# Optimization experiments

Hardware: AMD Instinct MI355X
Metric: run time of the kernel (lower is better)

Reference implementation:

```python
import jax, jax.numpy as jnp
import numpy as np

NH = 8       # num attention heads (hardcoded in module)
NL = 6       # n_layers
EPS = 1e-5   # LayerNorm eps (torch default)


def pos_enc(dim, length):
    # faithful to module's positional_encoding: even cols sin, odd cols cos,
    # with angle = pos / 10000^(2i/dim) where i indexes ALL columns via arange(0,2*dim,2)/dim
    pos = jnp.arange(length, dtype=jnp.float32)[:, None]
    div = 1.0 / (10000.0 ** (jnp.arange(0, 2 * dim, 2, dtype=jnp.float32) / dim))
    ang = pos * div[None, :]  # [length, dim]
    cols = jnp.arange(dim)
    return jnp.where(cols % 2 == 0, jnp.sin(ang), jnp.cos(ang))


def layernorm(x):
    m = x.mean(-1, keepdims=True)
    v = x.var(-1, keepdims=True)  # biased, matches torch LayerNorm
    return (x - m) / jnp.sqrt(v + EPS)


def setup_inputs() -> dict:
    key = jax.random.key(0)
    ks = jax.random.split(key, 8)
    S, H = 2048, 1024
    D = H // NH
    sc = 1.0 / np.sqrt(H)  # ~ torch Linear init scale
    return {
        "inputs": jax.random.normal(ks[0], (S, H), jnp.float32),
        "Wq": jax.random.normal(ks[1], (NH, H, D), jnp.float32) * sc,
        "bq": jnp.zeros((NH, D), jnp.float32),
        "Wk": jax.random.normal(ks[2], (NH, H, D), jnp.float32) * sc,
        "bk": jnp.zeros((NH, D), jnp.float32),
        "Wv": jax.random.normal(ks[3], (NH, H, D), jnp.float32) * sc,
        "bv": jnp.zeros((NH, D), jnp.float32),
        "W1": jax.random.normal(ks[4], (H, H), jnp.float32) * sc,
        "b1": jnp.zeros((H,), jnp.float32),
        "W2": jax.random.normal(ks[5], (H, H), jnp.float32) * sc,
        "b2": jnp.zeros((H,), jnp.float32),
    }


def reference(inputs, Wq, bq, Wk, bk, Wv, bv, W1, b1, W2, b2):
    S, H = inputs.shape
    scale = jnp.sqrt(jnp.float32(H))  # module scales by sqrt(hidden), not sqrt(head_dim)
    x = inputs + pos_enc(H, S)        # [S, H]
    kv = x  # dropout in eval mode = identity; k_v_input fixed to layer-0 input (faithful)
    # K/V are identical every layer (shared weights + fixed kv input)
    K = jnp.einsum('sh,nhd->nsd', kv, Wk) + bk[:, None, :]  # [NH, S, D]
    V = jnp.einsum('sh,nhd->nsd', kv, Wv) + bv[:, None, :]
    t_in = x
    for _ in range(NL):
        Q = jnp.einsum('sh,nhd->nsd', t_in, Wq) + bq[:, None, :]
        A = jax.nn.softmax(jnp.einsum('nsd,ntd->nst', Q, K) / scale, axis=-1)
        ctx = jnp.einsum('nst,ntd->nsd', A, V)        # [NH, S, D]
        cat = ctx.transpose(1, 0, 2).reshape(S, H)    # concat heads on feature dim
        mh = layernorm(t_in + cat)
        ff = jax.nn.relu(mh @ W1 + b1) @ W2 + b2
        t_in = layernorm(mh + ff)
    return t_in
```

## Files before the change

kernel.cpp:

```cpp
#include <hip/hip_runtime.h>

#define S_LEN 2048
#define H_DIM 1024
#define NHEAD 8
#define D_HEAD 128
#define KSPLIT 4
#define KV_PER (S_LEN / KSPLIT)

typedef __bf16 bf16x8 __attribute__((ext_vector_type(8)));
typedef float floatx4 __attribute__((ext_vector_type(4)));

__device__ __forceinline__ float b2f(unsigned short u) {
    union { unsigned int i; float f; } v;
    v.i = ((unsigned int)u) << 16;
    return v.f;
}
__device__ __forceinline__ unsigned short f2b(float f) {
    union { float f; unsigned int i; } v;
    v.f = f;
    return (unsigned short)((v.i + 0x7fffu + ((v.i >> 16) & 1u)) >> 16);
}

__device__ __forceinline__ void dma16(void* lds, const void* g) {
    __builtin_amdgcn_global_load_lds(
        (const __attribute__((address_space(1))) void*)g,
        (__attribute__((address_space(3))) void*)lds, 16, 0, 0);
}

__global__ __launch_bounds__(256) void posenc_kernel(
    const float* __restrict__ in, float* __restrict__ xf,
    unsigned short* __restrict__ xb)
{
    int g = blockIdx.x * 256 + threadIdx.x;
    int s = g >> 10;
    int h = g & 1023;
    float dv = powf(10000.0f, -(float)h * (1.0f / 512.0f));
    float ang = (float)s * dv;
    float pe = (h & 1) ? cosf(ang) : sinf(ang);
    float x = in[g] + pe;
    xf[g] = x;
    xb[g] = f2b(x);
}

__global__ __launch_bounds__(256) void transpose_f2b(
    const float* __restrict__ in, unsigned short* __restrict__ out, int R, int C)
{
    __shared__ unsigned short tile[32][33];
    const float* ih = in + (size_t)blockIdx.z * R * C;
    unsigned short* oh = out + (size_t)blockIdx.z * R * C;
    int r0 = blockIdx.y * 32, c0 = blockIdx.x * 32;
    int tx = threadIdx.x, ty = threadIdx.y;
    for (int i = ty; i < 32; i += 8)
        tile[i][tx] = f2b(ih[(size_t)(r0 + i) * C + c0 + tx]);
    __syncthreads();
    for (int i = ty; i < 32; i += 8)
        oh[(size_t)(c0 + i) * R + r0 + tx] = tile[tx][i];
}

template <int MODE, bool RELU>
__global__ __launch_bounds__(256, 4) void gemm_bt(
    const unsigned short* __restrict__ A, const unsigned short* __restrict__ Bt,
    const float* __restrict__ bias, float* __restrict__ Cf,
    unsigned short* __restrict__ Cb, int M, int N, int K, int ldt)
{
    __shared__ __align__(16) unsigned short sA[2][64 * 64];
    __shared__ __align__(16) unsigned short sB[2][64 * 64];
    const int tid = threadIdx.x;
    const int wave = tid >> 6, lane = tid & 63;
    const int quad = lane >> 4, l16 = lane & 15;
    const int i0 = blockIdx.y * 64, j0 = blockIdx.x * 64;
    const int wm = (wave >> 1) * 32, wn = (wave & 1) * 32;

    const int srow = lane >> 3;
    const int schunk = (lane & 7) ^ (srow & 7);
    const unsigned short* Ap0 = A + (size_t)(i0 + wave * 8 + srow) * K + schunk * 8;
    const unsigned short* Ap1 = A + (size_t)(i0 + 32 + wave * 8 + srow) * K + schunk * 8;
    const unsigned short* Bp0 = Bt + (size_t)(j0 + wave * 8 + srow) * K + schunk * 8;
    const unsigned short* Bp1 = Bt + (size_t)(j0 + 32 + wave * 8 + srow) * K + schunk * 8;
    const int ld0 = (wave * 8) * 64, ld1 = (32 + wave * 8) * 64;

    floatx4 z4 = {0.f, 0.f, 0.f, 0.f};
    floatx4 acc[2][2];
#pragma unroll
    for (int i = 0; i < 2; i++)
#pragma unroll
        for (int j = 0; j < 2; j++) acc[i][j] = z4;

    dma16(sA[0] + ld0, Ap0);
    dma16(sA[0] + ld1, Ap1);
    dma16(sB[0] + ld0, Bp0);
    dma16(sB[0] + ld1, Bp1);
    __syncthreads();

    int buf = 0;
    for (int k0 = 0; k0 < K; k0 += 64) {
        if (k0 + 64 < K) {
            dma16(sA[buf ^ 1] + ld0, Ap0 + k0 + 64);
            dma16(sA[buf ^ 1] + ld1, Ap1 + k0 + 64);
            dma16(sB[buf ^ 1] + ld0, Bp0 + k0 + 64);
            dma16(sB[buf ^ 1] + ld1, Bp1 + k0 + 64);
        }
        const unsigned short* cA = sA[buf];
        const unsigned short* cB = sB[buf];
#pragma unroll
        for (int kh = 0; kh < 2; kh++) {
            bf16x8 af[2], bfr[2];
#pragma unroll
            for (int mi = 0; mi < 2; mi++) {
                int row = wm + mi * 16 + l16;
                int p = (kh * 4 + quad) ^ (l16 & 7);
                af[mi] = *(const bf16x8*)(cA + row * 64 + p * 8);
            }
#pragma unroll
            for (int ni = 0; ni < 2; ni++) {
                int row = wn + ni * 16 + l16;
                int p = (kh * 4 + quad) ^ (l16 & 7);
                bfr[ni] = *(const bf16x8*)(cB + row * 64 + p * 8);
            }
#pragma unroll
            for (int mi = 0; mi < 2; mi++)
#pragma unroll
                for (int ni = 0; ni < 2; ni++)
                    acc[mi][ni] = __builtin_amdgcn_mfma_f32_16x16x32_bf16(
                        af[mi], bfr[ni], acc[mi][ni], 0, 0, 0);
        }
        __syncthreads();
        buf ^= 1;
    }

#pragma unroll
    for (int mi = 0; mi < 2; mi++) {
#pragma unroll
        for (int ni = 0; ni < 2; ni++) {
            const int col = j0 + wn + ni * 16 + l16;
            const float bval = bias[col];
#pragma unroll
            for (int r = 0; r < 4; r++) {
                const int row_o = i0 + wm + mi * 16 + quad * 4 + r;
                float v = acc[mi][ni][r] + bval;
                if (RELU) v = fmaxf(v, 0.0f);
                if (MODE == 0) Cb[(size_t)row_o * N + col] = f2b(v);
                else if (MODE == 1) Cb[(size_t)col * ldt + row_o] = f2b(v);
                else Cf[(size_t)row_o * N + col] = v;
            }
        }
    }
}

__global__ __launch_bounds__(256, 3) void flash_attn(
    const unsigned short* __restrict__ Qg, const unsigned short* __restrict__ Kg,
    const unsigned short* __restrict__ Vt, unsigned short* __restrict__ Op,
    float* __restrict__ Lp)
{
    __shared__ __align__(16) unsigned short sK[64 * 128];
    __shared__ __align__(16) unsigned short sV[128 * 64];

    const int tid = threadIdx.x;
    const int wave = tid >> 6, lane = tid & 63;
    const int quad = lane >> 4, l16 = lane & 15;
    const int head = blockIdx.y;
    const int q0 = blockIdx.x * 64;
    const int split = blockIdx.z;
    const int h0 = head * D_HEAD;

    bf16x8 aq[4];
    const int qrow = q0 + wave * 16 + l16;
#pragma unroll
    for (int ks = 0; ks < 4; ks++)
        aq[ks] = *(const bf16x8*)(Qg + (size_t)qrow * H_DIM + h0 + ks * 32 + quad * 8);

    unsigned short* myP = sK + wave * (16 * 72);

    const int k_r = wave * 4 + (lane >> 4);
    const int k_c = (lane & 15) ^ (k_r & 15);
    const int v_r = wave * 8 + (lane >> 3);
    const int v_c = (lane & 7) ^ (v_r & 7);

    const unsigned short* Kbase = Kg + h0;
    const unsigned short* Vbase = Vt + (size_t)h0 * S_LEN;
    const int kt0 = split * KV_PER;

    floatx4 z4 = {0.f, 0.f, 0.f, 0.f};
    floatx4 o[8];
#pragma unroll
    for (int i = 0; i < 8; i++) o[i] = z4;
    float l_r[4] = {0.f, 0.f, 0.f, 0.f};

    for (int it0 = 0; it0 < KV_PER; it0 += 64) {
        const int t0 = kt0 + it0;
        __syncthreads();
#pragma unroll
        for (int it = 0; it < 4; it++) {
            dma16(sK + (wave * 4 + it * 16) * 128,
                  Kbase + (size_t)(t0 + k_r + it * 16) * H_DIM + k_c * 8);
            dma16(sV + (wave * 8 + it * 32) * 64,
                  Vbase + (size_t)(v_r + it * 32) * S_LEN + t0 + v_c * 8);
        }
        __syncthreads();

        floatx4 sc[4];
#pragma unroll
        for (int ni = 0; ni < 4; ni++) {
            sc[ni] = z4;
#pragma unroll
            for (int ks = 0; ks < 4; ks++) {
                int p = (ks * 4 + quad) ^ l16;
                bf16x8 bk = *(const bf16x8*)(sK + (ni * 16 + l16) * 128 + p * 8);
                sc[ni] = __builtin_amdgcn_mfma_f32_16x16x32_bf16(aq[ks], bk, sc[ni], 0, 0, 0);
            }
        }

#pragma unroll
        for (int ni = 0; ni < 4; ni++)
#pragma unroll
            for (int r = 0; r < 4; r++) {
                float p = __expf(sc[ni][r] * 0.03125f);
                sc[ni][r] = p;
                l_r[r] += p;
            }

        __syncthreads();
#pragma unroll
        for (int ni = 0; ni < 4; ni++)
#pragma unroll
            for (int r = 0; r < 4; r++) {
                int prow = quad * 4 + r;
                myP[prow * 72 + ((ni * 16 + l16) ^ ((prow & 8) << 1))] = f2b(sc[ni][r]);
            }
        bf16x8 ap[2];
#pragma unroll
        for (int ks = 0; ks < 2; ks++)
            ap[ks] = *(const bf16x8*)(myP + l16 * 72 + ((ks * 32 + quad * 8) ^ ((l16 & 8) << 1)));
#pragma unroll
        for (int ni = 0; ni < 8; ni++) {
#pragma unroll
            for (int ks = 0; ks < 2; ks++) {
                int p = (ks * 4 + quad) ^ (l16 & 7);
                bf16x8 bv = *(const bf16x8*)(sV + (ni * 16 + l16) * 64 + p * 8);
                o[ni] = __builtin_amdgcn_mfma_f32_16x16x32_bf16(ap[ks], bv, o[ni], 0, 0, 0);
            }
        }
    }

#pragma unroll
    for (int r = 0; r < 4; r++)
#pragma unroll
        for (int off = 1; off < 16; off <<= 1)
            l_r[r] += __shfl_xor(l_r[r], off, 64);

#pragma unroll
    for (int r = 0; r < 4; r++) {
        float inv = 1.0f / l_r[r];
        int row = q0 + wave * 16 + quad * 4 + r;
#pragma unroll
        for (int ni = 0; ni < 8; ni++)
            Op[((size_t)split * S_LEN + row) * H_DIM + h0 + ni * 16 + l16] =
                f2b(o[ni][r] * inv);
        if (l16 == 0)
            Lp[(split * NHEAD + head) * S_LEN + row] = l_r[r];
    }
}

__global__ __launch_bounds__(256) void merge_add_layernorm(
    const float* __restrict__ t, const unsigned short* __restrict__ Op,
    const float* __restrict__ Lp,
    float* __restrict__ of, unsigned short* __restrict__ ob)
{
    __shared__ float red[8];
    const int row = blockIdx.x, tid = threadIdx.x;
    const int head = tid >> 5;
    const size_t base = (size_t)row * H_DIM + tid * 4;

    float l_s[KSPLIT];
    ushort4 os[KSPLIT];
#pragma unroll
    for (int sp = 0; sp < KSPLIT; sp++) {
        os[sp] = *(const ushort4*)(Op + ((size_t)sp * S_LEN + row) * H_DIM + tid * 4);
        l_s[sp] = Lp[(sp * NHEAD + head) * S_LEN + row];
    }
    float W = 0.f, a0 = 0.f, a1 = 0.f, a2 = 0.f, a3 = 0.f;
#pragma unroll
    for (int sp = 0; sp < KSPLIT; sp++) {
        float w = l_s[sp];
        W += w;
        a0 += w * b2f(os[sp].x);
        a1 += w * b2f(os[sp].y);
        a2 += w * b2f(os[sp].z);
        a3 += w * b2f(os[sp].w);
    }
    float inv = 1.0f / W;
    float4 x = *(const float4*)(t + base);
    float v0 = x.x + a0 * inv, v1 = x.y + a1 * inv;
    float v2 = x.z + a2 * inv, v3 = x.w + a3 * inv;

    float s = v0 + v1 + v2 + v3;
    float q = v0 * v0 + v1 * v1 + v2 * v2 + v3 * v3;
#pragma unroll
    for (int off = 32; off >= 1; off >>= 1) {
        s += __shfl_xor(s, off, 64);
        q += __shfl_xor(q, off, 64);
    }
    if ((tid & 63) == 0) { red[tid >> 6] = s; red[4 + (tid >> 6)] = q; }
    __syncthreads();
    s = red[0] + red[1] + red[2] + red[3];
    q = red[4] + red[5] + red[6] + red[7];
    const float mean = s * (1.0f / (float)H_DIM);
    const float var = q * (1.0f / (float)H_DIM) - mean * mean;
    const float rstd = rsqrtf(var + 1e-5f);
    float o0 = (v0 - mean) * rstd, o1 = (v1 - mean) * rstd;
    float o2 = (v2 - mean) * rstd, o3 = (v3 - mean) * rstd;
    *(float4*)(of + base) = make_float4(o0, o1, o2, o3);
    *(ushort4*)(ob + base) = make_ushort4(f2b(o0), f2b(o1), f2b(o2), f2b(o3));
}

__global__ __launch_bounds__(256) void add_layernorm(
    const float* __restrict__ a, const float* __restrict__ b,
    float* __restrict__ of, unsigned short* __restrict__ ob)
{
    __shared__ float red[8];
    const int row = blockIdx.x, tid = threadIdx.x;
    const size_t base = (size_t)row * H_DIM + tid * 4;
    float4 x = *(const float4*)(a + base);
    float4 y = *(const float4*)(b + base);
    float v0 = x.x + y.x, v1 = x.y + y.y, v2 = x.z + y.z, v3 = x.w + y.w;
    float s = v0 + v1 + v2 + v3;
    float q = v0 * v0 + v1 * v1 + v2 * v2 + v3 * v3;
#pragma unroll
    for (int off = 32; off >= 1; off >>= 1) {
        s += __shfl_xor(s, off, 64);
        q += __shfl_xor(q, off, 64);
    }
    if ((tid & 63) == 0) { red[tid >> 6] = s; red[4 + (tid >> 6)] = q; }
    __syncthreads();
    s = red[0] + red[1] + red[2] + red[3];
    q = red[4] + red[5] + red[6] + red[7];
    const float mean = s * (1.0f / (float)H_DIM);
    const float var = q * (1.0f / (float)H_DIM) - mean * mean;
    const float rstd = rsqrtf(var + 1e-5f);
    float o0 = (v0 - mean) * rstd, o1 = (v1 - mean) * rstd;
    float o2 = (v2 - mean) * rstd, o3 = (v3 - mean) * rstd;
    *(float4*)(of + base) = make_float4(o0, o1, o2, o3);
    *(ushort4*)(ob + base) = make_ushort4(f2b(o0), f2b(o1), f2b(o2), f2b(o3));
}

extern "C" void kernel_launch(void* const* d_in, const int* in_sizes, int n_in,
                              void* d_out, int out_size, void* d_ws, size_t ws_size,
                              hipStream_t stream)
{
    (void)in_sizes; (void)n_in; (void)out_size; (void)ws_size;
    const float* in = (const float*)d_in[0];
    const float* Wq = (const float*)d_in[1];
    const float* bq = (const float*)d_in[2];
    const float* Wk = (const float*)d_in[3];
    const float* bk = (const float*)d_in[4];
    const float* Wv = (const float*)d_in[5];
    const float* bv = (const float*)d_in[6];
    const float* W1 = (const float*)d_in[7];
    const float* b1 = (const float*)d_in[8];
    const float* W2 = (const float*)d_in[9];
    const float* b2 = (const float*)d_in[10];

    char* ws = (char*)d_ws;
    const size_t MB = 1024 * 1024;
    float* t_f32 = (float*)(ws + 0 * MB);
    float* cf_f32 = (float*)(ws + 8 * MB);
    unsigned short* t_b = (unsigned short*)(ws + 16 * MB);
    unsigned short* K_b = (unsigned short*)(ws + 20 * MB);
    unsigned short* Vt_b = (unsigned short*)(ws + 24 * MB);
    unsigned short* Q_b = (unsigned short*)(ws + 28 * MB);
    unsigned short* WqT = (unsigned short*)(ws + 32 * MB);
    unsigned short* WkT = (unsigned short*)(ws + 34 * MB);
    unsigned short* WvT = (unsigned short*)(ws + 36 * MB);
    unsigned short* W1T = (unsigned short*)(ws + 38 * MB);
    unsigned short* W2T = (unsigned short*)(ws + 40 * MB);
    unsigned short* Op = (unsigned short*)(ws + 42 * MB);
    float* Lp = (float*)(ws + 58 * MB);

    dim3 tb(32, 8);
    transpose_f2b<<<dim3(4, 32, 8), tb, 0, stream>>>(Wq, WqT, H_DIM, D_HEAD);
    transpose_f2b<<<dim3(4, 32, 8), tb, 0, stream>>>(Wk, WkT, H_DIM, D_HEAD);
    transpose_f2b<<<dim3(4, 32, 8), tb, 0, stream>>>(Wv, WvT, H_DIM, D_HEAD);
    transpose_f2b<<<dim3(32, 32, 1), tb, 0, stream>>>(W1, W1T, H_DIM, H_DIM);
    transpose_f2b<<<dim3(32, 32, 1), tb, 0, stream>>>(W2, W2T, H_DIM, H_DIM);

    posenc_kernel<<<(S_LEN * H_DIM) / 256, 256, 0, stream>>>(in, t_f32, t_b);

    dim3 gg(H_DIM / 64, S_LEN / 64);
    gemm_bt<0, false><<<gg, 256, 0, stream>>>(t_b, WkT, bk, nullptr, K_b, S_LEN, H_DIM, H_DIM, 0);
    gemm_bt<1, false><<<gg, 256, 0, stream>>>(t_b, WvT, bv, nullptr, Vt_b, S_LEN, H_DIM, H_DIM, S_LEN);

    for (int layer = 0; layer < 6; layer++) {
        gemm_bt<0, false><<<gg, 256, 0, stream>>>(t_b, WqT, bq, nullptr, Q_b, S_LEN, H_DIM, H_DIM, 0);
        flash_attn<<<dim3(S_LEN / 64, NHEAD, KSPLIT), 256, 0, stream>>>(Q_b, K_b, Vt_b, Op, Lp);
        merge_add_layernorm<<<S_LEN, 256, 0, stream>>>(t_f32, Op, Lp, t_f32, t_b);
        gemm_bt<0, true><<<gg, 256, 0, stream>>>(t_b, W1T, b1, nullptr, Q_b, S_LEN, H_DIM, H_DIM, 0);
        gemm_bt<2, false><<<gg, 256, 0, stream>>>(Q_b, W2T, b2, cf_f32, nullptr, S_LEN, H_DIM, H_DIM, 0);
        float* of = (layer == 5) ? (float*)d_out : t_f32;
        add_layernorm<<<S_LEN, 256, 0, stream>>>(t_f32, cf_f32, of, t_b);
    }
}
```

Before: 633.0 us.

## Process two 16-row query tiles per wave in flash attention to reuse K/V tiles

Each wave now handles 32 query rows instead of 16, so a block covers 128 queries, and every K/V fragment read from LDS feeds two MFMAs. The grid halves along the query dimension. P now goes to its own LDS buffer instead of aliasing sK, which removes one __syncthreads per KV tile. In exchange, register pressure roughly doubles for accumulators, occupancy drops from 3 to 2 blocks per CU, there are fewer blocks (512) to fill the GPU, and LDS use per block grows.

```diff
diff --git a/kernel.cpp b/kernel.cpp
--- a/kernel.cpp
+++ b/kernel.cpp
@@ -147,29 +147,33 @@
     }
 }
 
-__global__ __launch_bounds__(256, 3) void flash_attn(
+__global__ __launch_bounds__(256, 2) void flash_attn(
     const unsigned short* __restrict__ Qg, const unsigned short* __restrict__ Kg,
     const unsigned short* __restrict__ Vt, unsigned short* __restrict__ Op,
     float* __restrict__ Lp)
 {
     __shared__ __align__(16) unsigned short sK[64 * 128];
     __shared__ __align__(16) unsigned short sV[128 * 64];
+    __shared__ __align__(16) unsigned short sP[4 * 32 * 72];
 
     const int tid = threadIdx.x;
     const int wave = tid >> 6, lane = tid & 63;
     const int quad = lane >> 4, l16 = lane & 15;
     const int head = blockIdx.y;
-    const int q0 = blockIdx.x * 64;
+    const int q0 = blockIdx.x * 128;
     const int split = blockIdx.z;
     const int h0 = head * D_HEAD;
 
-    bf16x8 aq[4];
-    const int qrow = q0 + wave * 16 + l16;
-#pragma unroll
-    for (int ks = 0; ks < 4; ks++)
-        aq[ks] = *(const bf16x8*)(Qg + (size_t)qrow * H_DIM + h0 + ks * 32 + quad * 8);
-
-    unsigned short* myP = sK + wave * (16 * 72);
+    bf16x8 aq[2][4];
+#pragma unroll
+    for (int m = 0; m < 2; m++) {
+        const int qrow = q0 + wave * 32 + m * 16 + l16;
+#pragma unroll
+        for (int ks = 0; ks < 4; ks++)
+            aq[m][ks] = *(const bf16x8*)(Qg + (size_t)qrow * H_DIM + h0 + ks * 32 + quad * 8);
+    }
+
+    unsigned short* myP = sP + wave * (32 * 72);
 
     const int k_r = wave * 4 + (lane >> 4);
     const int k_c = (lane & 15) ^ (k_r & 15);
@@ -181,10 +185,12 @@
     const int kt0 = split * KV_PER;
 
     floatx4 z4 = {0.f, 0.f, 0.f, 0.f};
-    floatx4 o[8];
-#pragma unroll
-    for (int i = 0; i < 8; i++) o[i] = z4;
-    float l_r[4] = {0.f, 0.f, 0.f, 0.f};
+    floatx4 o[2][8];
+#pragma unroll
+    for (int m = 0; m < 2; m++)
+#pragma unroll
+        for (int i = 0; i < 8; i++) o[m][i] = z4;
+    float l_r[2][4] = {{0.f, 0.f, 0.f, 0.f}, {0.f, 0.f, 0.f, 0.f}};
 
     for (int it0 = 0; it0 < KV_PER; it0 += 64) {
         const int t0 = kt0 + it0;
@@ -198,67 +204,86 @@
         }
         __syncthreads();
 
-        floatx4 sc[4];
+        floatx4 sc[2][4];
+#pragma unroll
+        for (int m = 0; m < 2; m++)
+#pragma unroll
+            for (int ni = 0; ni < 4; ni++) sc[m][ni] = z4;
 #pragma unroll
         for (int ni = 0; ni < 4; ni++) {
-            sc[ni] = z4;
 #pragma unroll
             for (int ks = 0; ks < 4; ks++) {
                 int p = (ks * 4 + quad) ^ l16;
                 bf16x8 bk = *(const bf16x8*)(sK + (ni * 16 + l16) * 128 + p * 8);
-                sc[ni] = __builtin_amdgcn_mfma_f32_16x16x32_bf16(aq[ks], bk, sc[ni], 0, 0, 0);
+#pragma unroll
+                for (int m = 0; m < 2; m++)
+                    sc[m][ni] = __builtin_amdgcn_mfma_f32_16x16x32_bf16(
+                        aq[m][ks], bk, sc[m][ni], 0, 0, 0);
             }
         }
 
 #pragma unroll
-        for (int ni = 0; ni < 4; ni++)
-#pragma unroll
-            for (int r = 0; r < 4; r++) {
-                float p = __expf(sc[ni][r] * 0.03125f);
-                sc[ni][r] = p;
-                l_r[r] += p;
-            }
-
-        __syncthreads();
-#pragma unroll
-        for (int ni = 0; ni < 4; ni++)
-#pragma unroll
-            for (int r = 0; r < 4; r++) {
-                int prow = quad * 4 + r;
-                myP[prow * 72 + ((ni * 16 + l16) ^ ((prow & 8) << 1))] = f2b(sc[ni][r]);
-            }
-        bf16x8 ap[2];
-#pragma unroll
-        for (int ks = 0; ks < 2; ks++)
-            ap[ks] = *(const bf16x8*)(myP + l16 * 72 + ((ks * 32 + quad * 8) ^ ((l16 & 8) << 1)));
+        for (int m = 0; m < 2; m++)
+#pragma unroll
+            for (int ni = 0; ni < 4; ni++)
+#pragma unroll
+                for (int r = 0; r < 4; r++) {
+                    float p = __expf(sc[m][ni][r] * 0.03125f);
+                    sc[m][ni][r] = p;
+                    l_r[m][r] += p;
+                }
+
+#pragma unroll
+        for (int m = 0; m < 2; m++)
+#pragma unroll
+            for (int ni = 0; ni < 4; ni++)
+#pragma unroll
+                for (int r = 0; r < 4; r++) {
+                    int prow = m * 16 + quad * 4 + r;
+                    myP[prow * 72 + ((ni * 16 + l16) ^ ((prow & 8) << 1))] = f2b(sc[m][ni][r]);
+                }
+        bf16x8 ap[2][2];
+#pragma unroll
+        for (int m = 0; m < 2; m++)
+#pragma unroll
+            for (int ks = 0; ks < 2; ks++)
+                ap[m][ks] = *(const bf16x8*)(myP + (m * 16 + l16) * 72 +
+                                             ((ks * 32 + quad * 8) ^ ((l16 & 8) << 1)));
 #pragma unroll
         for (int ni = 0; ni < 8; ni++) {
 #pragma unroll
             for (int ks = 0; ks < 2; ks++) {
                 int p = (ks * 4 + quad) ^ (l16 & 7);
                 bf16x8 bv = *(const bf16x8*)(sV + (ni * 16 + l16) * 64 + p * 8);
-                o[ni] = __builtin_amdgcn_mfma_f32_16x16x32_bf16(ap[ks], bv, o[ni], 0, 0, 0);
+#pragma unroll
+                for (int m = 0; m < 2; m++)
+                    o[m][ni] = __builtin_amdgcn_mfma_f32_16x16x32_bf16(
+                        ap[m][ks], bv, o[m][ni], 0, 0, 0);
             }
         }
     }
 
 #pragma unroll
-    for (int r = 0; r < 4; r++)
-#pragma unroll
-        for (int off = 1; off < 16; off <<= 1)
-            l_r[r] += __shfl_xor(l_r[r], off, 64);
-
-#pragma unroll
-    for (int r = 0; r < 4; r++) {
-        float inv = 1.0f / l_r[r];
-        int row = q0 + wave * 16 + quad * 4 + r;
-#pragma unroll
-        for (int ni = 0; ni < 8; ni++)
-            Op[((size_t)split * S_LEN + row) * H_DIM + h0 + ni * 16 + l16] =
-                f2b(o[ni][r] * inv);
-        if (l16 == 0)
-            Lp[(split * NHEAD + head) * S_LEN + row] = l_r[r];
-    }
+    for (int m = 0; m < 2; m++)
+#pragma unroll
+        for (int r = 0; r < 4; r++)
+#pragma unroll
+            for (int off = 1; off < 16; off <<= 1)
+                l_r[m][r] += __shfl_xor(l_r[m][r], off, 64);
+
+#pragma unroll
+    for (int m = 0; m < 2; m++)
+#pragma unroll
+        for (int r = 0; r < 4; r++) {
+            float inv = 1.0f / l_r[m][r];
+            int row = q0 + wave * 32 + m * 16 + quad * 4 + r;
+#pragma unroll
+            for (int ni = 0; ni < 8; ni++)
+                Op[((size_t)split * S_LEN + row) * H_DIM + h0 + ni * 16 + l16] =
+                    f2b(o[m][ni][r] * inv);
+            if (l16 == 0)
+                Lp[(split * NHEAD + head) * S_LEN + row] = l_r[m][r];
+        }
 }
 
 __global__ __launch_bounds__(256) void merge_add_layernorm(
@@ -391,7 +416,7 @@
 
     for (int layer = 0; layer < 6; layer++) {
         gemm_bt<0, false><<<gg, 256, 0, stream>>>(t_b, WqT, bq, nullptr, Q_b, S_LEN, H_DIM, H_DIM, 0);
-        flash_attn<<<dim3(S_LEN / 64, NHEAD, KSPLIT), 256, 0, stream>>>(Q_b, K_b, Vt_b, Op, Lp);
+        flash_attn<<<dim3(S_LEN / 128, NHEAD, KSPLIT), 256, 0, stream>>>(Q_b, K_b, Vt_b, Op, Lp);
         merge_add_layernorm<<<S_LEN, 256, 0, stream>>>(t_f32, Op, Lp, t_f32, t_b);
         gemm_bt<0, true><<<gg, 256, 0, stream>>>(t_b, W1T, b1, nullptr, Q_b, S_LEN, H_DIM, H_DIM, 0);
         gemm_bt<2, false><<<gg, 256, 0, stream>>>(Q_b, W2T, b2, cf_f32, nullptr, S_LEN, H_DIM, H_DIM, 0);
```

Result: no change. 630.3 us (-0.4%).

## Double-buffer V tiles in LDS and load K fragments directly from global

Applied to the files above, without the earlier changes.

The flash attention kernel now stages V tiles into two LDS buffers, prefetching the next tile while computing on the current one, and leaves one barrier per iteration. K is no longer staged in LDS: each wave reads its K fragments straight from global memory into registers. P gets its own LDS region. This aims to hide load latency and cut barriers. The cost is redundant global K reads across the four waves and uncoalesced row-strided accesses.

```diff
diff --git a/kernel.cpp b/kernel.cpp
--- a/kernel.cpp
+++ b/kernel.cpp
@@ -152,8 +152,8 @@
     const unsigned short* __restrict__ Vt, unsigned short* __restrict__ Op,
     float* __restrict__ Lp)
 {
-    __shared__ __align__(16) unsigned short sK[64 * 128];
-    __shared__ __align__(16) unsigned short sV[128 * 64];
+    __shared__ __align__(16) unsigned short sV[2][128 * 64];
+    __shared__ __align__(16) unsigned short sP[4 * 16 * 72];
 
     const int tid = threadIdx.x;
     const int wave = tid >> 6, lane = tid & 63;
@@ -169,10 +169,8 @@
     for (int ks = 0; ks < 4; ks++)
         aq[ks] = *(const bf16x8*)(Qg + (size_t)qrow * H_DIM + h0 + ks * 32 + quad * 8);
 
-    unsigned short* myP = sK + wave * (16 * 72);
-
-    const int k_r = wave * 4 + (lane >> 4);
-    const int k_c = (lane & 15) ^ (k_r & 15);
+    unsigned short* myP = sP + wave * (16 * 72);
+
     const int v_r = wave * 8 + (lane >> 3);
     const int v_c = (lane & 7) ^ (v_r & 7);
 
@@ -186,28 +184,35 @@
     for (int i = 0; i < 8; i++) o[i] = z4;
     float l_r[4] = {0.f, 0.f, 0.f, 0.f};
 
+#pragma unroll
+    for (int it = 0; it < 4; it++)
+        dma16(sV[0] + (wave * 8 + it * 32) * 64,
+              Vbase + (size_t)(v_r + it * 32) * S_LEN + kt0 + v_c * 8);
+    __syncthreads();
+
+    int buf = 0;
     for (int it0 = 0; it0 < KV_PER; it0 += 64) {
         const int t0 = kt0 + it0;
-        __syncthreads();
-#pragma unroll
-        for (int it = 0; it < 4; it++) {
-            dma16(sK + (wave * 4 + it * 16) * 128,
-                  Kbase + (size_t)(t0 + k_r + it * 16) * H_DIM + k_c * 8);
-            dma16(sV + (wave * 8 + it * 32) * 64,
-                  Vbase + (size_t)(v_r + it * 32) * S_LEN + t0 + v_c * 8);
-        }
-        __syncthreads();
+        if (it0 + 64 < KV_PER) {
+            const int nt = t0 + 64;
+#pragma unroll
+            for (int it = 0; it < 4; it++)
+                dma16(sV[buf ^ 1] + (wave * 8 + it * 32) * 64,
+                      Vbase + (size_t)(v_r + it * 32) * S_LEN + nt + v_c * 8);
+        }
 
         floatx4 sc[4];
 #pragma unroll
         for (int ni = 0; ni < 4; ni++) {
+            bf16x8 bkf[4];
+#pragma unroll
+            for (int ks = 0; ks < 4; ks++)
+                bkf[ks] = *(const bf16x8*)(Kbase +
+                    (size_t)(t0 + ni * 16 + l16) * H_DIM + ks * 32 + quad * 8);
             sc[ni] = z4;
 #pragma unroll
-            for (int ks = 0; ks < 4; ks++) {
-                int p = (ks * 4 + quad) ^ l16;
-                bf16x8 bk = *(const bf16x8*)(sK + (ni * 16 + l16) * 128 + p * 8);
-                sc[ni] = __builtin_amdgcn_mfma_f32_16x16x32_bf16(aq[ks], bk, sc[ni], 0, 0, 0);
-            }
+            for (int ks = 0; ks < 4; ks++)
+                sc[ni] = __builtin_amdgcn_mfma_f32_16x16x32_bf16(aq[ks], bkf[ks], sc[ni], 0, 0, 0);
         }
 
 #pragma unroll
@@ -219,7 +224,6 @@
                 l_r[r] += p;
             }
 
-        __syncthreads();
 #pragma unroll
         for (int ni = 0; ni < 4; ni++)
 #pragma unroll
@@ -231,15 +235,19 @@
 #pragma unroll
         for (int ks = 0; ks < 2; ks++)
             ap[ks] = *(const bf16x8*)(myP + l16 * 72 + ((ks * 32 + quad * 8) ^ ((l16 & 8) << 1)));
+
 #pragma unroll
         for (int ni = 0; ni < 8; ni++) {
 #pragma unroll
             for (int ks = 0; ks < 2; ks++) {
                 int p = (ks * 4 + quad) ^ (l16 & 7);
-                bf16x8 bv = *(const bf16x8*)(sV + (ni * 16 + l16) * 64 + p * 8);
+                bf16x8 bv = *(const bf16x8*)(sV[buf] + (ni * 16 + l16) * 64 + p * 8);
                 o[ni] = __builtin_amdgcn_mfma_f32_16x16x32_bf16(ap[ks], bv, o[ni], 0, 0, 0);
             }
         }
+
+        __syncthreads();
+        buf ^= 1;
     }
 
 #pragma unroll
```

After: 976.7 us. +54.3%, slower.

## Double-buffer K/V tiles in flash attention with smaller 32-key tiles

Applied to the files above, without the earlier changes.

Restructures the flash attention inner loop to prefetch the next K/V tile into a second LDS buffer while computing on the current one. The KV tile shrinks from 64 to 32 keys so that two buffers fit, and a dedicated P scratch buffer replaces the reuse of sK. This cuts the per-iteration barrier count from three to one and overlaps global-to-LDS DMA with MFMA work. In exchange there are twice as many loop iterations, and the async DMA now relies on the end-of-loop barrier for completion.

```diff
diff --git a/kernel.cpp b/kernel.cpp
--- a/kernel.cpp
+++ b/kernel.cpp
@@ -152,8 +152,9 @@
     const unsigned short* __restrict__ Vt, unsigned short* __restrict__ Op,
     float* __restrict__ Lp)
 {
-    __shared__ __align__(16) unsigned short sK[64 * 128];
-    __shared__ __align__(16) unsigned short sV[128 * 64];
+    __shared__ __align__(16) unsigned short sK[2][32 * 128];
+    __shared__ __align__(16) unsigned short sV[2][128 * 32];
+    __shared__ __align__(16) unsigned short sP[4 * 16 * 40];
 
     const int tid = threadIdx.x;
     const int wave = tid >> 6, lane = tid & 63;
@@ -169,12 +170,12 @@
     for (int ks = 0; ks < 4; ks++)
         aq[ks] = *(const bf16x8*)(Qg + (size_t)qrow * H_DIM + h0 + ks * 32 + quad * 8);
 
-    unsigned short* myP = sK + wave * (16 * 72);
+    unsigned short* myP = sP + wave * (16 * 40);
 
     const int k_r = wave * 4 + (lane >> 4);
     const int k_c = (lane & 15) ^ (k_r & 15);
-    const int v_r = wave * 8 + (lane >> 3);
-    const int v_c = (lane & 7) ^ (v_r & 7);
+    const int v_r = wave * 16 + (lane >> 2);
+    const int v_c = (lane & 3) ^ (v_r & 3);
 
     const unsigned short* Kbase = Kg + h0;
     const unsigned short* Vbase = Vt + (size_t)h0 * S_LEN;
@@ -186,32 +187,42 @@
     for (int i = 0; i < 8; i++) o[i] = z4;
     float l_r[4] = {0.f, 0.f, 0.f, 0.f};
 
-    for (int it0 = 0; it0 < KV_PER; it0 += 64) {
-        const int t0 = kt0 + it0;
-        __syncthreads();
-#pragma unroll
-        for (int it = 0; it < 4; it++) {
-            dma16(sK + (wave * 4 + it * 16) * 128,
-                  Kbase + (size_t)(t0 + k_r + it * 16) * H_DIM + k_c * 8);
-            dma16(sV + (wave * 8 + it * 32) * 64,
-                  Vbase + (size_t)(v_r + it * 32) * S_LEN + t0 + v_c * 8);
-        }
-        __syncthreads();
-
-        floatx4 sc[4];
-#pragma unroll
-        for (int ni = 0; ni < 4; ni++) {
+#pragma unroll
+    for (int it = 0; it < 2; it++) {
+        dma16(sK[0] + (it * 16 + wave * 4) * 128,
+              Kbase + (size_t)(kt0 + k_r + it * 16) * H_DIM + k_c * 8);
+        dma16(sV[0] + (it * 64 + wave * 16) * 32,
+              Vbase + (size_t)(v_r + it * 64) * S_LEN + kt0 + v_c * 8);
+    }
+    __syncthreads();
+
+    int buf = 0;
+    for (int it0 = 0; it0 < KV_PER; it0 += 32) {
+        if (it0 + 32 < KV_PER) {
+            const int nt = kt0 + it0 + 32;
+#pragma unroll
+            for (int it = 0; it < 2; it++) {
+                dma16(sK[buf ^ 1] + (it * 16 + wave * 4) * 128,
+                      Kbase + (size_t)(nt + k_r + it * 16) * H_DIM + k_c * 8);
+                dma16(sV[buf ^ 1] + (it * 64 + wave * 16) * 32,
+                      Vbase + (size_t)(v_r + it * 64) * S_LEN + nt + v_c * 8);
+            }
+        }
+
+        floatx4 sc[2];
+#pragma unroll
+        for (int ni = 0; ni < 2; ni++) {
             sc[ni] = z4;
 #pragma unroll
             for (int ks = 0; ks < 4; ks++) {
                 int p = (ks * 4 + quad) ^ l16;
-                bf16x8 bk = *(const bf16x8*)(sK + (ni * 16 + l16) * 128 + p * 8);
+                bf16x8 bk = *(const bf16x8*)(sK[buf] + (ni * 16 + l16) * 128 + p * 8);
                 sc[ni] = __builtin_amdgcn_mfma_f32_16x16x32_bf16(aq[ks], bk, sc[ni], 0, 0, 0);
             }
         }
 
 #pragma unroll
-        for (int ni = 0; ni < 4; ni++)
+        for (int ni = 0; ni < 2; ni++)
 #pragma unroll
             for (int r = 0; r < 4; r++) {
                 float p = __expf(sc[ni][r] * 0.03125f);
@@ -219,27 +230,24 @@
                 l_r[r] += p;
             }
 
-        __syncthreads();
-#pragma unroll
-        for (int ni = 0; ni < 4; ni++)
+#pragma unroll
+        for (int ni = 0; ni < 2; ni++)
 #pragma unroll
             for (int r = 0; r < 4; r++) {
                 int prow = quad * 4 + r;
-                myP[prow * 72 + ((ni * 16 + l16) ^ ((prow & 8) << 1))] = f2b(sc[ni][r]);
-            }
-        bf16x8 ap[2];
-#pragma unroll
-        for (int ks = 0; ks < 2; ks++)
-            ap[ks] = *(const bf16x8*)(myP + l16 * 72 + ((ks * 32 + quad * 8) ^ ((l16 & 8) << 1)));
+                myP[prow * 40 + ((ni * 16 + l16) ^ ((prow & 8) << 1))] = f2b(sc[ni][r]);
+            }
+        bf16x8 ap = *(const bf16x8*)(myP + l16 * 40 + ((quad * 8) ^ ((l16 & 8) << 1)));
+
 #pragma unroll
         for (int ni = 0; ni < 8; ni++) {
-#pragma unroll
-            for (int ks = 0; ks < 2; ks++) {
-                int p = (ks * 4 + quad) ^ (l16 & 7);
-                bf16x8 bv = *(const bf16x8*)(sV + (ni * 16 + l16) * 64 + p * 8);
-                o[ni] = __builtin_amdgcn_mfma_f32_16x16x32_bf16(ap[ks], bv, o[ni], 0, 0, 0);
-            }
-        }
+            int p = quad ^ (l16 & 3);
+            bf16x8 bv = *(const bf16x8*)(sV[buf] + (ni * 16 + l16) * 32 + p * 8);
+            o[ni] = __builtin_amdgcn_mfma_f32_16x16x32_bf16(ap, bv, o[ni], 0, 0, 0);
+        }
+
+        __syncthreads();
+        buf ^= 1;
     }
 
 #pragma unroll
```

Measured after the change: 639.5 us. Within noise of the previous version (+1.0%).
